# Optimization experiments

Measured on AMD Instinct MI355X. Metric: run time of the kernel, lower is better.

## Reference

```python
import jax, jax.numpy as jnp
import numpy as np

B, S, D, H = 2, 2048, 1024, 16
HD = D // H  # head_size = 64

def setup_inputs() -> dict:
    key = jax.random.key(0)
    ks = jax.random.split(key, 8)
    sc = 0.02
    return {
        "q": jax.random.normal(ks[0], (B, S, D), jnp.float32),
        "k": jax.random.normal(ks[1], (B, S, D), jnp.float32),
        "v": jax.random.normal(ks[2], (B, S, D), jnp.float32),
        "padding_mask": jnp.zeros((B, 1, 1, S), jnp.float32),
        "Wq": jax.random.normal(ks[3], (D, D), jnp.float32) * sc,
        "bq": jnp.zeros((D,), jnp.float32),
        "Wk": jax.random.normal(ks[4], (D, D), jnp.float32) * sc,
        "bk": jnp.zeros((D,), jnp.float32),
        "Wv": jax.random.normal(ks[5], (D, D), jnp.float32) * sc,
        "bv": jnp.zeros((D,), jnp.float32),
        "Wo": jax.random.normal(ks[6], (D, D), jnp.float32) * sc,
        "bo": jnp.zeros((D,), jnp.float32),
    }

def reference(q, k, v, padding_mask, Wq, bq, Wk, bk, Wv, bv, Wo, bo):
    b = q.shape[0]
    qh = (q @ Wq + bq).reshape(b, -1, H, HD)
    kh = (k @ Wk + bk).reshape(b, -1, H, HD)
    vh = (v @ Wv + bv).reshape(b, -1, H, HD)
    # [B, H, Sq, Sk] scores, materialized as in the original
    qk = jnp.einsum('bjhd,bkhd->bhjk', qh, kh) / jnp.sqrt(jnp.float32(HD))
    qk = qk + padding_mask * -1e12
    attn = jax.nn.softmax(qk, axis=-1)
    qkv = jnp.einsum('bhjk,bkhd->bjhd', attn, vh).reshape(b, -1, D)
    return qkv @ Wo + bo
```

## Files before the change

### kernel.cpp

```cpp
#include <hip/hip_runtime.h>
#include <math.h>

typedef __bf16 bf16_t;
typedef __bf16 bf16x8 __attribute__((ext_vector_type(8)));
typedef __bf16 bf16x4v __attribute__((ext_vector_type(4)));
typedef float f32x4 __attribute__((ext_vector_type(4)));
typedef float f32x16 __attribute__((ext_vector_type(16)));

#define LOG2E 1.4426950408889634f
#define MBIAS_C (-1e12f * LOG2E)

#if __has_builtin(__builtin_amdgcn_exp2f)
#define EXP2F(x) __builtin_amdgcn_exp2f(x)
#else
#define EXP2F(x) exp2f(x)
#endif

typedef __attribute__((address_space(1))) const unsigned int g_u32;
typedef __attribute__((address_space(3))) unsigned int l_u32;
__device__ __forceinline__ void load_lds_16B(const void* g, void* l){
  __builtin_amdgcn_global_load_lds((g_u32*)g, (l_u32*)l, 16, 0, 0);
}

__device__ __forceinline__ f32x16 zero16(){
  f32x16 z;
  #pragma unroll
  for (int i = 0; i < 16; i++) z[i] = 0.f;
  return z;
}

typedef union { bf16x4v b4; uint2 u2; } pk8;
typedef union { uint2 h[2]; bf16x8 b8; } pk16;

__global__ __launch_bounds__(256) void cast3_kernel(const float* __restrict__ q,
                                                    const float* __restrict__ k,
                                                    const float* __restrict__ v,
                                                    bf16_t* __restrict__ out){
  int z = blockIdx.y;
  const float* x = (z == 0) ? q : (z == 1) ? k : v;
  int i = blockIdx.x * 256 + threadIdx.x;
  float4 f = reinterpret_cast<const float4*>(x)[i];
  bf16x4v w;
  w[0] = (bf16_t)f.x; w[1] = (bf16_t)f.y; w[2] = (bf16_t)f.z; w[3] = (bf16_t)f.w;
  reinterpret_cast<bf16x4v*>(out + (size_t)z * 4194304)[i] = w;
}

__global__ __launch_bounds__(256) void wtrans4_kernel(const float* __restrict__ Wq,
                                                      const float* __restrict__ Wk,
                                                      const float* __restrict__ Wv,
                                                      const float* __restrict__ Wo,
                                                      bf16_t* __restrict__ Wcat,
                                                      bf16_t* __restrict__ Wot){
  __shared__ float T[32][33];
  int z = blockIdx.z;
  const float* W = (z == 0) ? Wq : (z == 1) ? Wk : (z == 2) ? Wv : Wo;
  bf16_t* dst = (z < 3) ? (Wcat + (size_t)z * 1024 * 1024) : Wot;
  int x = threadIdx.x, y = threadIdx.y;
  int k0 = blockIdx.y * 32, n0 = blockIdx.x * 32;
  #pragma unroll
  for (int i = 0; i < 4; i++) T[y + 8*i][x] = W[(size_t)(k0 + y + 8*i) * 1024 + n0 + x];
  __syncthreads();
  #pragma unroll
  for (int i = 0; i < 4; i++) dst[(size_t)(n0 + y + 8*i) * 1024 + k0 + x] = (bf16_t)T[x][y + 8*i];
}

__device__ __forceinline__ void qkv_epilogue(f32x4 (&acc)[4][4], int seg, int n0g, int m0,
                                             int wm, int wn, int l16, int lq,
                                             const float* bias, bf16_t* qp, bf16_t* kp,
                                             bf16_t* vh){
  bf16_t* Cp = (seg == 0) ? qp : (seg == 1) ? kp : vh;
  float scale = (seg == 0) ? 0.125f * LOG2E : 1.0f;
  #pragma unroll
  for (int ti = 0; ti < 4; ti++){
    #pragma unroll
    for (int tj = 0; tj < 4; tj++){
      int col = (n0g + wn + tj*16 + l16) & 1023;
      float bvv = bias[col];
      #pragma unroll
      for (int r = 0; r < 4; r++){
        int row = m0 + wm + ti*16 + lq*4 + r;
        Cp[(size_t)row * 1024 + col] = (bf16_t)((acc[ti][tj][r] + bvv) * scale);
      }
    }
  }
}

__global__ __launch_bounds__(256) void gemm_qkv_bf(const bf16_t* __restrict__ qkvin,
                                                   const bf16_t* __restrict__ Wcat,
                                                   const float* __restrict__ bq,
                                                   const float* __restrict__ bk,
                                                   const float* __restrict__ bv,
                                                   bf16_t* __restrict__ qp,
                                                   bf16_t* __restrict__ kp,
                                                   bf16_t* __restrict__ vh){
  const int K = 1024;
  __shared__ __align__(16) bf16_t As[128*32];
  __shared__ __align__(16) bf16_t Bs[128*32];
  int tid = threadIdx.x, wave = tid >> 6, lane = tid & 63;
  int l16 = lane & 15, lq = lane >> 4;
  int n0g = blockIdx.x * 128;
  int seg = n0g >> 10;
  const bf16_t* A   = qkvin + (size_t)seg * 4194304;
  const float* bias = (seg == 0) ? bq : (seg == 1) ? bk : bv;
  int m0 = blockIdx.y * 128;
  int wm = (wave >> 1) * 64, wn = (wave & 1) * 64;
  int cposR = lq ^ ((l16 >> 2) & 3);
  f32x4 acc[4][4] = {};
  for (int kt = 0; kt < K; kt += 32){
    __syncthreads();
    #pragma unroll
    for (int i = 0; i < 2; i++){
      int u = tid + 256*i;
      int r = u >> 2, cpos = u & 3, cg = cpos ^ ((r >> 2) & 3);
      int ldsoff = (wave*64 + 256*i) * 16;
      load_lds_16B(&A[(size_t)(m0 + r) * K + kt + cg*8], (char*)As + ldsoff);
      load_lds_16B(&Wcat[(size_t)(n0g + r) * K + kt + cg*8], (char*)Bs + ldsoff);
    }
    __syncthreads();
    bf16x8 af[4], bfr[4];
    #pragma unroll
    for (int t = 0; t < 4; t++) af[t]  = *reinterpret_cast<bf16x8*>(&As[(wm + t*16 + l16)*32 + cposR*8]);
    #pragma unroll
    for (int t = 0; t < 4; t++) bfr[t] = *reinterpret_cast<bf16x8*>(&Bs[(wn + t*16 + l16)*32 + cposR*8]);
    #pragma unroll
    for (int ti = 0; ti < 4; ti++)
      #pragma unroll
      for (int tj = 0; tj < 4; tj++)
        acc[ti][tj] = __builtin_amdgcn_mfma_f32_16x16x32_bf16(af[ti], bfr[tj], acc[ti][tj], 0, 0, 0);
  }
  qkv_epilogue(acc, seg, n0g, m0, wm, wn, l16, lq, bias, qp, kp, vh);
}

__global__ __launch_bounds__(256) void gemm_qkv_f32(const float* __restrict__ qi,
                                                    const float* __restrict__ ki,
                                                    const float* __restrict__ vi,
                                                    const bf16_t* __restrict__ Wcat,
                                                    const float* __restrict__ bq,
                                                    const float* __restrict__ bk,
                                                    const float* __restrict__ bv,
                                                    bf16_t* __restrict__ qp,
                                                    bf16_t* __restrict__ kp,
                                                    bf16_t* __restrict__ vh){
  const int K = 1024;
  __shared__ __align__(16) float  Asf[128*32];
  __shared__ __align__(16) bf16_t Bs[128*32];
  int tid = threadIdx.x, wave = tid >> 6, lane = tid & 63;
  int l16 = lane & 15, lq = lane >> 4;
  int n0g = blockIdx.x * 128;
  int seg = n0g >> 10;
  const float* A    = (seg == 0) ? qi : (seg == 1) ? ki : vi;
  const float* bias = (seg == 0) ? bq : (seg == 1) ? bk : bv;
  int m0 = blockIdx.y * 128;
  int wm = (wave >> 1) * 64, wn = (wave & 1) * 64;
  int cposR = lq ^ ((l16 >> 2) & 3);
  int ca0 = (2*lq)     ^ (l16 & 7);
  int ca1 = (2*lq + 1) ^ (l16 & 7);
  f32x4 acc[4][4] = {};
  for (int kt = 0; kt < K; kt += 32){
    __syncthreads();
    #pragma unroll
    for (int i = 0; i < 4; i++){
      int u = tid + 256*i;
      int r = u >> 3, cpos = u & 7, cg = cpos ^ (r & 7);
      load_lds_16B(&A[(size_t)(m0 + r) * K + kt + cg*4], (char*)Asf + (wave*64 + 256*i)*16);
    }
    #pragma unroll
    for (int i = 0; i < 2; i++){
      int u = tid + 256*i;
      int r = u >> 2, cpos = u & 3, cg = cpos ^ ((r >> 2) & 3);
      load_lds_16B(&Wcat[(size_t)(n0g + r) * K + kt + cg*8], (char*)Bs + (wave*64 + 256*i)*16);
    }
    __syncthreads();
    bf16x8 af[4], bfr[4];
    #pragma unroll
    for (int t = 0; t < 4; t++){
      int row = wm + t*16 + l16;
      f32x4 x0 = *reinterpret_cast<f32x4*>(&Asf[row*32 + ca0*4]);
      f32x4 x1 = *reinterpret_cast<f32x4*>(&Asf[row*32 + ca1*4]);
      bf16x8 a;
      a[0] = (bf16_t)x0[0]; a[1] = (bf16_t)x0[1]; a[2] = (bf16_t)x0[2]; a[3] = (bf16_t)x0[3];
      a[4] = (bf16_t)x1[0]; a[5] = (bf16_t)x1[1]; a[6] = (bf16_t)x1[2]; a[7] = (bf16_t)x1[3];
      af[t] = a;
    }
    #pragma unroll
    for (int t = 0; t < 4; t++) bfr[t] = *reinterpret_cast<bf16x8*>(&Bs[(wn + t*16 + l16)*32 + cposR*8]);
    #pragma unroll
    for (int ti = 0; ti < 4; ti++)
      #pragma unroll
      for (int tj = 0; tj < 4; tj++)
        acc[ti][tj] = __builtin_amdgcn_mfma_f32_16x16x32_bf16(af[ti], bfr[tj], acc[ti][tj], 0, 0, 0);
  }
  qkv_epilogue(acc, seg, n0g, m0, wm, wn, l16, lq, bias, qp, kp, vh);
}

__global__ __launch_bounds__(256) void gemm_out(const bf16_t* __restrict__ A,
                                                const bf16_t* __restrict__ Bt,
                                                const float* __restrict__ bias,
                                                float* __restrict__ C){
  const int K = 1024, N = 1024;
  __shared__ __align__(16) bf16_t As[128*64];
  __shared__ __align__(16) bf16_t Bs[64*64];
  int tid = threadIdx.x, wave = tid >> 6, lane = tid & 63;
  int l16 = lane & 15, lq = lane >> 4;
  int m0 = blockIdx.y * 128, n0 = blockIdx.x * 64;
  int wm = wave * 32;
  f32x4 acc[2][4] = {};
  for (int kt = 0; kt < K; kt += 64){
    __syncthreads();
    #pragma unroll
    for (int i = 0; i < 4; i++){
      int u = tid + 256*i;
      int r = u >> 3, cpos = u & 7, cg = cpos ^ (r & 7);
      load_lds_16B(&A[(size_t)(m0 + r) * K + kt + cg*8], (char*)As + (wave*64 + 256*i)*16);
    }
    #pragma unroll
    for (int i = 0; i < 2; i++){
      int u = tid + 256*i;
      int r = u >> 3, cpos = u & 7, cg = cpos ^ (r & 7);
      load_lds_16B(&Bt[(size_t)(n0 + r) * K + kt + cg*8], (char*)Bs + (wave*64 + 256*i)*16);
    }
    __syncthreads();
    #pragma unroll
    for (int kk = 0; kk < 2; kk++){
      bf16x8 af[2], bfr[4];
      #pragma unroll
      for (int t = 0; t < 2; t++){
        int row = wm + t*16 + l16, cpos = (kk*4 + lq) ^ (l16 & 7);
        af[t] = *reinterpret_cast<bf16x8*>(&As[row*64 + cpos*8]);
      }
      #pragma unroll
      for (int t = 0; t < 4; t++){
        int row = t*16 + l16, cpos = (kk*4 + lq) ^ (l16 & 7);
        bfr[t] = *reinterpret_cast<bf16x8*>(&Bs[row*64 + cpos*8]);
      }
      #pragma unroll
      for (int ti = 0; ti < 2; ti++)
        #pragma unroll
        for (int tj = 0; tj < 4; tj++)
          acc[ti][tj] = __builtin_amdgcn_mfma_f32_16x16x32_bf16(af[ti], bfr[tj], acc[ti][tj], 0, 0, 0);
    }
  }
  #pragma unroll
  for (int ti = 0; ti < 2; ti++){
    #pragma unroll
    for (int tj = 0; tj < 4; tj++){
      int col = n0 + tj*16 + l16;
      float bvv = bias[col];
      #pragma unroll
      for (int r = 0; r < 4; r++){
        int row = m0 + wm + ti*16 + lq*4 + r;
        C[(size_t)row * N + col] = acc[ti][tj][r] + bvv;
      }
    }
  }
}

__global__ __launch_bounds__(256) void vtrans_kernel(const bf16_t* __restrict__ vh,
                                                     bf16_t* __restrict__ Vt){
  __shared__ bf16_t T[64][72];
  int tid = threadIdx.x;
  int s0 = blockIdx.x * 64, h = blockIdx.y, b = blockIdx.z;
  #pragma unroll
  for (int i = 0; i < 2; i++){
    int u = tid + 256*i;
    int r = u >> 3, c = (u & 7) * 8;
    *reinterpret_cast<uint4*>(&T[r][c]) =
      *reinterpret_cast<const uint4*>(&vh[(size_t)(b*2048 + s0 + r) * 1024 + h*64 + c]);
  }
  __syncthreads();
  #pragma unroll
  for (int i = 0; i < 2; i++){
    int u = tid + 256*i;
    int d = u >> 3, cs = (u & 7) * 8;
    bf16_t t8[8];
    #pragma unroll
    for (int j = 0; j < 8; j++) t8[j] = T[cs + j][d];
    *reinterpret_cast<uint4*>(&Vt[(size_t)((b*16 + h)*64 + d) * 2048 + s0 + cs]) =
      *reinterpret_cast<uint4*>(t8);
  }
}

__global__ __launch_bounds__(256) void attn_kernel(const bf16_t* __restrict__ qp,
                                                   const bf16_t* __restrict__ kp,
                                                   const bf16_t* __restrict__ vt,
                                                   const float* __restrict__ mask,
                                                   bf16_t* __restrict__ ctx){
  const int S = 2048, D = 1024, HD = 64;
  __shared__ __align__(16) char smem[16896];
  bf16_t* Ks  = (bf16_t*)smem;
  bf16_t* Vts = (bf16_t*)(smem + 8192);
  float* Lbuf = (float*)(smem + 16384);
  int tid = threadIdx.x, wave = tid >> 6, lane = tid & 63;
  int l32 = lane & 31, H = lane >> 5;
  int qt = blockIdx.x, h = blockIdx.y, b = blockIdx.z;
  const bf16_t* Qg = qp + (size_t)b*S*D + h*HD;
  const bf16_t* Kg = kp + (size_t)b*S*D + h*HD;
  const bf16_t* Vg = vt + (size_t)(b*16 + h)*HD*S;

  int qrow = qt*128 + wave*32 + l32;
  bf16x8 qf[4];
  #pragma unroll
  for (int s = 0; s < 4; s++)
    qf[s] = *reinterpret_cast<const bf16x8*>(&Qg[(size_t)qrow * D + s*16 + 8*H]);

  f32x16 o0 = zero16(), o1 = zero16();
  float lacc = 0.f;

  for (int kt = 0; kt < S; kt += 64){
    __syncthreads();
    #pragma unroll
    for (int i = 0; i < 2; i++){
      int u = tid + 256*i;
      int r = u >> 3, c = u & 7, cg = c ^ (r & 7);
      load_lds_16B(&Kg[(size_t)(kt + r) * D + cg*8], (char*)Ks + (wave*64 + 256*i)*16);
    }
    #pragma unroll
    for (int i = 0; i < 2; i++){
      int u = tid + 256*i;
      int r = u >> 3, c = u & 7, cg = c ^ (r & 7);
      load_lds_16B(&Vg[(size_t)r * S + kt + cg*8], (char*)Vts + (wave*64 + 256*i)*16);
    }
    __syncthreads();

    f32x16 sc0, sc1;
    #pragma unroll
    for (int s = 0; s < 4; s++){
      int cp = (2*s + H) ^ (l32 & 7);
      bf16x8 kf0 = *reinterpret_cast<bf16x8*>(&Ks[l32*64 + cp*8]);
      bf16x8 kf1 = *reinterpret_cast<bf16x8*>(&Ks[(32 + l32)*64 + cp*8]);
      if (s == 0){
        sc0 = __builtin_amdgcn_mfma_f32_32x32x16_bf16(kf0, qf[0], zero16(), 0, 0, 0);
        sc1 = __builtin_amdgcn_mfma_f32_32x32x16_bf16(kf1, qf[0], zero16(), 0, 0, 0);
      } else {
        sc0 = __builtin_amdgcn_mfma_f32_32x32x16_bf16(kf0, qf[s], sc0, 0, 0, 0);
        sc1 = __builtin_amdgcn_mfma_f32_32x32x16_bf16(kf1, qf[s], sc1, 0, 0, 0);
      }
    }
    pk8 grp[2][4];
    #pragma unroll
    for (int t = 0; t < 2; t++){
      const f32x16& s = t ? sc1 : sc0;
      #pragma unroll
      for (int g = 0; g < 4; g++){
        int kcol = kt + t*32 + 8*g + 4*H;
        float4 mv = *reinterpret_cast<const float4*>(&mask[(size_t)b*S + kcol]);
        float p0 = EXP2F(fmaf(mv.x, MBIAS_C, s[4*g+0]));
        float p1 = EXP2F(fmaf(mv.y, MBIAS_C, s[4*g+1]));
        float p2 = EXP2F(fmaf(mv.z, MBIAS_C, s[4*g+2]));
        float p3 = EXP2F(fmaf(mv.w, MBIAS_C, s[4*g+3]));
        lacc += (p0 + p1) + (p2 + p3);
        pk8 w;
        w.b4[0] = (bf16_t)p0; w.b4[1] = (bf16_t)p1; w.b4[2] = (bf16_t)p2; w.b4[3] = (bf16_t)p3;
        grp[t][g] = w;
      }
    }
    #pragma unroll
    for (int kk = 0; kk < 4; kk++){
      int t = kk >> 1, w = kk & 1;
      uint2 ga = grp[t][2*w].u2;
      uint2 gb = grp[t][2*w+1].u2;
      uint2 send = H ? ga : gb;
      uint2 recv;
      recv.x = (unsigned)__shfl_xor((int)send.x, 32);
      recv.y = (unsigned)__shfl_xor((int)send.y, 32);
      pk16 fr;
      fr.h[0] = H ? recv : ga;
      fr.h[1] = H ? gb : recv;
      int cp = (2*kk + H) ^ (l32 & 7);
      bf16x8 vf0 = *reinterpret_cast<bf16x8*>(&Vts[l32*64 + cp*8]);
      bf16x8 vf1 = *reinterpret_cast<bf16x8*>(&Vts[(32 + l32)*64 + cp*8]);
      o0 = __builtin_amdgcn_mfma_f32_32x32x16_bf16(fr.b8, vf0, o0, 0, 0, 0);
      o1 = __builtin_amdgcn_mfma_f32_32x32x16_bf16(fr.b8, vf1, o1, 0, 0, 0);
    }
  }
  float lfull = lacc + __shfl_xor(lacc, 32);
  Lbuf[wave*32 + l32] = lfull;
  #pragma unroll
  for (int g = 0; g < 4; g++){
    f32x4 lv = *reinterpret_cast<f32x4*>(&Lbuf[wave*32 + 8*g + 4*H]);
    #pragma unroll
    for (int r = 0; r < 4; r++){
      float inv = 1.f / lv[r];
      int grow = qt*128 + wave*32 + 8*g + 4*H + r;
      size_t base = (size_t)(b*S + grow) * D + h*HD;
      ctx[base + l32]      = (bf16_t)(o0[4*g + r] * inv);
      ctx[base + 32 + l32] = (bf16_t)(o1[4*g + r] * inv);
    }
  }
}

extern "C" void kernel_launch(void* const* d_in, const int* in_sizes, int n_in,
                              void* d_out, int out_size, void* d_ws, size_t ws_size,
                              hipStream_t stream){
  const float* q    = (const float*)d_in[0];
  const float* k    = (const float*)d_in[1];
  const float* v    = (const float*)d_in[2];
  const float* mask = (const float*)d_in[3];
  const float* Wq   = (const float*)d_in[4];
  const float* bq   = (const float*)d_in[5];
  const float* Wk   = (const float*)d_in[6];
  const float* bk   = (const float*)d_in[7];
  const float* Wv   = (const float*)d_in[8];
  const float* bv   = (const float*)d_in[9];
  const float* Wo   = (const float*)d_in[10];
  const float* bo   = (const float*)d_in[11];

  char* ws = (char*)d_ws;
  bf16_t* qp    = (bf16_t*)(ws);
  bf16_t* kp    = (bf16_t*)(ws + 8388608);
  bf16_t* vh    = (bf16_t*)(ws + 16777216);
  bf16_t* Wcat  = (bf16_t*)(ws + 25165824);
  bf16_t* Wot   = (bf16_t*)(ws + 31457280);
  bf16_t* Vt    = (bf16_t*)(ws + 33554432);
  bf16_t* ctx   = (bf16_t*)(ws + 41943040);
  bf16_t* qkvin = (bf16_t*)(ws + 33554432);

  wtrans4_kernel<<<dim3(32,32,4), dim3(32,8), 0, stream>>>(Wq, Wk, Wv, Wo, Wcat, Wot);
  if (ws_size >= 58720256){
    cast3_kernel<<<dim3(4096,3), 256, 0, stream>>>(q, k, v, qkvin);
    gemm_qkv_bf<<<dim3(24,32), 256, 0, stream>>>(qkvin, Wcat, bq, bk, bv, qp, kp, vh);
  } else {
    gemm_qkv_f32<<<dim3(24,32), 256, 0, stream>>>(q, k, v, Wcat, bq, bk, bv, qp, kp, vh);
  }
  vtrans_kernel<<<dim3(32,16,2), 256, 0, stream>>>(vh, Vt);
  attn_kernel<<<dim3(16,16,2), 256, 0, stream>>>(qp, kp, Vt, mask, ctx);
  gemm_out<<<dim3(16,32), 256, 0, stream>>>(ctx, Wot, bo, (float*)d_out);
}
```

Before: 263.8 us.

## Split attention key tiles across waves and double the attention grid

```diff
diff --git a/kernel.cpp b/kernel.cpp
--- a/kernel.cpp
+++ b/kernel.cpp
@@ -286,18 +286,27 @@
                                                    const float* __restrict__ mask,
                                                    bf16_t* __restrict__ ctx){
   const int S = 2048, D = 1024, HD = 64;
-  __shared__ __align__(16) char smem[16896];
-  bf16_t* Ks  = (bf16_t*)smem;
-  bf16_t* Vts = (bf16_t*)(smem + 8192);
-  float* Lbuf = (float*)(smem + 16384);
+  __shared__ __align__(16) char smem[25216];
+  bf16_t* Ks   = (bf16_t*)smem;
+  bf16_t* Vts  = (bf16_t*)(smem + 8192);
+  float*  Mb   = (float*)(smem + 16384);
+  float*  Lsum = (float*)(smem + 24576);
+  float*  Lcomb= (float*)(smem + 24832);
+  float*  Opart= (float*)smem;
   int tid = threadIdx.x, wave = tid >> 6, lane = tid & 63;
   int l32 = lane & 31, H = lane >> 5;
+  int qhalf = wave & 1, khalf = wave >> 1;
   int qt = blockIdx.x, h = blockIdx.y, b = blockIdx.z;
   const bf16_t* Qg = qp + (size_t)b*S*D + h*HD;
   const bf16_t* Kg = kp + (size_t)b*S*D + h*HD;
   const bf16_t* Vg = vt + (size_t)(b*16 + h)*HD*S;
-
-  int qrow = qt*128 + wave*32 + l32;
+  const float*  Mg = mask + (size_t)b*S;
+
+  #pragma unroll
+  for (int i = 0; i < 2; i++)
+    load_lds_16B(&Mg[(tid + 256*i)*4], (char*)Mb + (wave*64 + 256*i)*16);
+
+  int qrow = qt*64 + qhalf*32 + l32;
   bf16x8 qf[4];
   #pragma unroll
   for (int s = 0; s < 4; s++)
@@ -305,6 +314,7 @@
 
   f32x16 o0 = zero16(), o1 = zero16();
   float lacc = 0.f;
+  int krow = khalf*32 + l32;
 
   for (int kt = 0; kt < S; kt += 64){
     __syncthreads();
@@ -322,43 +332,31 @@
     }
     __syncthreads();
 
-    f32x16 sc0, sc1;
+    f32x16 sc;
     #pragma unroll
     for (int s = 0; s < 4; s++){
       int cp = (2*s + H) ^ (l32 & 7);
-      bf16x8 kf0 = *reinterpret_cast<bf16x8*>(&Ks[l32*64 + cp*8]);
-      bf16x8 kf1 = *reinterpret_cast<bf16x8*>(&Ks[(32 + l32)*64 + cp*8]);
-      if (s == 0){
-        sc0 = __builtin_amdgcn_mfma_f32_32x32x16_bf16(kf0, qf[0], zero16(), 0, 0, 0);
-        sc1 = __builtin_amdgcn_mfma_f32_32x32x16_bf16(kf1, qf[0], zero16(), 0, 0, 0);
-      } else {
-        sc0 = __builtin_amdgcn_mfma_f32_32x32x16_bf16(kf0, qf[s], sc0, 0, 0, 0);
-        sc1 = __builtin_amdgcn_mfma_f32_32x32x16_bf16(kf1, qf[s], sc1, 0, 0, 0);
-      }
-    }
-    pk8 grp[2][4];
-    #pragma unroll
-    for (int t = 0; t < 2; t++){
-      const f32x16& s = t ? sc1 : sc0;
-      #pragma unroll
-      for (int g = 0; g < 4; g++){
-        int kcol = kt + t*32 + 8*g + 4*H;
-        float4 mv = *reinterpret_cast<const float4*>(&mask[(size_t)b*S + kcol]);
-        float p0 = EXP2F(fmaf(mv.x, MBIAS_C, s[4*g+0]));
-        float p1 = EXP2F(fmaf(mv.y, MBIAS_C, s[4*g+1]));
-        float p2 = EXP2F(fmaf(mv.z, MBIAS_C, s[4*g+2]));
-        float p3 = EXP2F(fmaf(mv.w, MBIAS_C, s[4*g+3]));
-        lacc += (p0 + p1) + (p2 + p3);
-        pk8 w;
-        w.b4[0] = (bf16_t)p0; w.b4[1] = (bf16_t)p1; w.b4[2] = (bf16_t)p2; w.b4[3] = (bf16_t)p3;
-        grp[t][g] = w;
-      }
-    }
-    #pragma unroll
-    for (int kk = 0; kk < 4; kk++){
-      int t = kk >> 1, w = kk & 1;
-      uint2 ga = grp[t][2*w].u2;
-      uint2 gb = grp[t][2*w+1].u2;
+      bf16x8 kf = *reinterpret_cast<bf16x8*>(&Ks[krow*64 + cp*8]);
+      if (s == 0) sc = __builtin_amdgcn_mfma_f32_32x32x16_bf16(kf, qf[0], zero16(), 0, 0, 0);
+      else        sc = __builtin_amdgcn_mfma_f32_32x32x16_bf16(kf, qf[s], sc, 0, 0, 0);
+    }
+    pk8 grp[4];
+    #pragma unroll
+    for (int g = 0; g < 4; g++){
+      float4 mv = *reinterpret_cast<float4*>(&Mb[kt + khalf*32 + 8*g + 4*H]);
+      float p0 = EXP2F(fmaf(mv.x, MBIAS_C, sc[4*g+0]));
+      float p1 = EXP2F(fmaf(mv.y, MBIAS_C, sc[4*g+1]));
+      float p2 = EXP2F(fmaf(mv.z, MBIAS_C, sc[4*g+2]));
+      float p3 = EXP2F(fmaf(mv.w, MBIAS_C, sc[4*g+3]));
+      lacc += (p0 + p1) + (p2 + p3);
+      pk8 w;
+      w.b4[0] = (bf16_t)p0; w.b4[1] = (bf16_t)p1; w.b4[2] = (bf16_t)p2; w.b4[3] = (bf16_t)p3;
+      grp[g] = w;
+    }
+    #pragma unroll
+    for (int kk = 0; kk < 2; kk++){
+      uint2 ga = grp[2*kk].u2;
+      uint2 gb = grp[2*kk+1].u2;
       uint2 send = H ? ga : gb;
       uint2 recv;
       recv.x = (unsigned)__shfl_xor((int)send.x, 32);
@@ -366,7 +364,7 @@
       pk16 fr;
       fr.h[0] = H ? recv : ga;
       fr.h[1] = H ? gb : recv;
-      int cp = (2*kk + H) ^ (l32 & 7);
+      int cp = (4*khalf + 2*kk + H) ^ (l32 & 7);
       bf16x8 vf0 = *reinterpret_cast<bf16x8*>(&Vts[l32*64 + cp*8]);
       bf16x8 vf1 = *reinterpret_cast<bf16x8*>(&Vts[(32 + l32)*64 + cp*8]);
       o0 = __builtin_amdgcn_mfma_f32_32x32x16_bf16(fr.b8, vf0, o0, 0, 0, 0);
@@ -374,17 +372,35 @@
     }
   }
   float lfull = lacc + __shfl_xor(lacc, 32);
-  Lbuf[wave*32 + l32] = lfull;
-  #pragma unroll
-  for (int g = 0; g < 4; g++){
-    f32x4 lv = *reinterpret_cast<f32x4*>(&Lbuf[wave*32 + 8*g + 4*H]);
-    #pragma unroll
-    for (int r = 0; r < 4; r++){
-      float inv = 1.f / lv[r];
-      int grow = qt*128 + wave*32 + 8*g + 4*H + r;
-      size_t base = (size_t)(b*S + grow) * D + h*HD;
-      ctx[base + l32]      = (bf16_t)(o0[4*g + r] * inv);
-      ctx[base + 32 + l32] = (bf16_t)(o1[4*g + r] * inv);
+  __syncthreads();
+  if (khalf == 1){
+    #pragma unroll
+    for (int reg = 0; reg < 16; reg++){
+      Opart[qhalf*2048 + reg*64 + lane]        = o0[reg];
+      Opart[qhalf*2048 + 1024 + reg*64 + lane] = o1[reg];
+    }
+    if (H == 0) Lsum[qhalf*32 + l32] = lfull;
+  }
+  __syncthreads();
+  if (khalf == 0){
+    #pragma unroll
+    for (int reg = 0; reg < 16; reg++){
+      o0[reg] += Opart[qhalf*2048 + reg*64 + lane];
+      o1[reg] += Opart[qhalf*2048 + 1024 + reg*64 + lane];
+    }
+    lfull += Lsum[qhalf*32 + l32];
+    Lcomb[qhalf*32 + l32] = lfull;
+    #pragma unroll
+    for (int g = 0; g < 4; g++){
+      f32x4 lv = *reinterpret_cast<f32x4*>(&Lcomb[qhalf*32 + 8*g + 4*H]);
+      #pragma unroll
+      for (int r = 0; r < 4; r++){
+        float inv = 1.f / lv[r];
+        int grow = qt*64 + qhalf*32 + 8*g + 4*H + r;
+        size_t base = (size_t)(b*S + grow) * D + h*HD;
+        ctx[base + l32]      = (bf16_t)(o0[4*g + r] * inv);
+        ctx[base + 32 + l32] = (bf16_t)(o1[4*g + r] * inv);
+      }
     }
   }
 }
@@ -423,6 +439,6 @@
     gemm_qkv_f32<<<dim3(24,32), 256, 0, stream>>>(q, k, v, Wcat, bq, bk, bv, qp, kp, vh);
   }
   vtrans_kernel<<<dim3(32,16,2), 256, 0, stream>>>(vh, Vt);
-  attn_kernel<<<dim3(16,16,2), 256, 0, stream>>>(qp, kp, Vt, mask, ctx);
+  attn_kernel<<<dim3(32,16,2), 256, 0, stream>>>(qp, kp, Vt, mask, ctx);
   gemm_out<<<dim3(16,32), 256, 0, stream>>>(ctx, Wot, bo, (float*)d_out);
 }
```

Result: faster. 241.7 us (-8.4%).
